# Kernel tuning notes

Hardware: AMD Instinct MI355X
Metric: run time of the kernel (lower is better)

The kernel has to match this reference:

```python
import jax, jax.numpy as jnp
import numpy as np

B, T, H, V = 256, 256, 512, 32000
L = 3  # stacked LSTM layers


def setup_inputs() -> dict:
    key = jax.random.key(0)
    ks = jax.random.split(key, 12)
    s = 0.05
    n = lambda k, shp: (jax.random.normal(k, shp, jnp.float32) * s)
    return {
        "text_1": jax.random.randint(ks[0], (B, T), 0, V, dtype=jnp.int32),
        "text_2": jax.random.randint(ks[1], (B, T), 0, V, dtype=jnp.int32),
        "text_3": jax.random.randint(ks[2], (B, T), 0, V, dtype=jnp.int32),
        "emb": n(ks[3], (V, H)),
        "Wx": n(ks[4], (L, H, 4 * H)),
        "Wh": n(ks[5], (L, H, 4 * H)),
        "b": jnp.zeros((L, 4 * H), jnp.float32),
        "g1": jnp.ones((3 * H,), jnp.float32), "beta1": jnp.zeros((3 * H,), jnp.float32),
        "W1": n(ks[6], (3 * H, 2 * H)), "bd1": jnp.zeros((2 * H,), jnp.float32),
        "g2": jnp.ones((2 * H,), jnp.float32), "beta2": jnp.zeros((2 * H,), jnp.float32),
        "W2": n(ks[7], (2 * H, H // 5)), "bd2": jnp.zeros((H // 5,), jnp.float32),
        "g3": jnp.ones((H // 5,), jnp.float32), "beta3": jnp.zeros((H // 5,), jnp.float32),
        "W3": n(ks[8], (H // 5, 4)), "bd3": jnp.zeros((4,), jnp.float32),
    }


def _lstm_stack(tokens, emb, Wx, Wh, b):
    # tokens: [B, T] int -> last hidden of top layer [B, H]
    x = emb[tokens]                      # [B, T, H]
    x = jnp.transpose(x, (1, 0, 2))      # [T, B, H] (scan over time)
    bsz, h = x.shape[1], Wh.shape[1]
    for l in range(Wx.shape[0]):
        Wx_l, Wh_l, b_l = Wx[l], Wh[l], b[l]
        def step(carry, xt):
            hprev, cprev = carry
            gates = xt @ Wx_l + hprev @ Wh_l + b_l      # [B, 4H]
            i, f, g, o = jnp.split(gates, 4, axis=-1)
            c = jax.nn.sigmoid(f) * cprev + jax.nn.sigmoid(i) * jnp.tanh(g)
            hnew = jax.nn.sigmoid(o) * jnp.tanh(c)
            return (hnew, c), hnew
        init = (jnp.zeros((bsz, h), x.dtype), jnp.zeros((bsz, h), x.dtype))
        _, x = jax.lax.scan(step, init, x)
    return x[-1]                          # rnn_output[:, -1, :]


def _bn(x, gamma, beta, eps=1e-3):
    m = jnp.mean(x, axis=0)
    v = jnp.var(x, axis=0)
    return gamma * (x - m) * jax.lax.rsqrt(v + eps) + beta


def reference(text_1, text_2, text_3, emb, Wx, Wh, b,
              g1, beta1, W1, bd1, g2, beta2, W2, bd2, g3, beta3, W3, bd3):
    r1 = _lstm_stack(text_1, emb, Wx, Wh, b)
    r2 = _lstm_stack(text_2, emb, Wx, Wh, b)
    r3 = _lstm_stack(text_3, emb, Wx, Wh, b)
    r = jnp.concatenate([r1, r2, r3], axis=1)   # [B, 3H]
    r = _bn(r, g1, beta1)
    r = jax.nn.selu(r @ W1 + bd1)
    r = _bn(r, g2, beta2)
    r = jax.nn.selu(r @ W2 + bd2)
    r = _bn(r, g3, beta3)
    return r @ W3 + bd3                          # [B, 4] logits
```

## Files before the change

### kernel.cpp

```cpp
#include <hip/hip_runtime.h>
#include <hip/hip_bf16.h>
#include <hip/hip_cooperative_groups.h>

namespace cg = cooperative_groups;

typedef __attribute__((ext_vector_type(8))) short short8;
typedef __attribute__((ext_vector_type(4))) float floatx4;

namespace {
constexpr int kB1 = 256;
constexpr int kT  = 256;
constexpr int kH  = 512;
constexpr int kL  = 3;
constexpr int kK  = 1024;
constexpr int kN  = 2048;
constexpr int kGrid = 576;
constexpr size_t kHB = (size_t)768 * kH;

constexpr size_t WREP_OFF   = 0;
constexpr size_t WREP_BYTES = (size_t)kL * kK * kN * 2;
constexpr size_t BREP_OFF   = WREP_OFF + WREP_BYTES;
constexpr size_t BREP_BYTES = (size_t)kL * kN * 4;
constexpr size_t HBUF_OFF   = BREP_OFF + BREP_BYTES;
constexpr size_t HBUF_BYTES = (size_t)kL * 2 * kHB * 2;
constexpr size_t CBUF_OFF   = HBUF_OFF + HBUF_BYTES;
constexpr size_t CBUF_BYTES = (size_t)kL * kHB * 4;
constexpr size_t BNA_OFF    = CBUF_OFF + CBUF_BYTES;
constexpr size_t BNC_OFF    = BNA_OFF + 1536 * 4;
constexpr size_t Z1_OFF     = BNC_OFF + 1536 * 4;
constexpr size_t Z2_OFF     = Z1_OFF + (size_t)256 * 1024 * 4;
constexpr size_t FLAG_OFF   = Z2_OFF + (size_t)256 * 102 * 4;
}

__device__ __forceinline__ float ldf(const void* p, size_t idx, int isf32) {
  if (isf32) return ((const float*)p)[idx];
  return __bfloat162float(((const __hip_bfloat16*)p)[idx]);
}

__device__ __forceinline__ short f2bs(float x) {
  union { __hip_bfloat16 h; short s; } u;
  u.h = __float2bfloat16(x);
  return u.s;
}

__device__ __forceinline__ float fast_tanh(float x) {
  float e = __expf(2.f * x);
  return __fdividef(e - 1.f, e + 1.f);
}
__device__ __forceinline__ float fast_sigmoid(float x) {
  return __fdividef(1.f, 1.f + __expf(-x));
}

__global__ void detect_kernel(const unsigned* __restrict__ g1, int* __restrict__ flag) {
  if (threadIdx.x == 0 && blockIdx.x == 0)
    *flag = (g1[0] == 0x3F800000u) ? 1 : 0;
}

__device__ __forceinline__ void repack_body(
    int start, int stride,
    const void* __restrict__ Wx, const void* __restrict__ Wh,
    const void* __restrict__ bias, int isf32,
    __hip_bfloat16* __restrict__ Wrep, float* __restrict__ brep) {
  for (int idx = start; idx < kL * kK * kN; idx += stride) {
    int j  = idx & 7;
    int n2 = (idx >> 3) & (kN - 1);
    int kg = (idx >> 14) & 127;
    int l  = idx >> 21;
    int k  = kg * 8 + j;
    int ntile = n2 >> 7, c = n2 & 127, g = c >> 5, ul = c & 31;
    int u = ntile * 32 + ul;
    int col = g * 512 + u;
    float v;
    if (k < kH) v = ldf(Wx, ((size_t)l * kH + k) * kN + col, isf32);
    else        v = ldf(Wh, ((size_t)l * kH + (k - kH)) * kN + col, isf32);
    Wrep[idx] = __float2bfloat16(v);
    if (kg == 0 && j == 0) brep[l * kN + n2] = ldf(bias, (size_t)l * kN + col, isf32);
  }
}

__global__ __launch_bounds__(256) void repack_kernel(
    const void* __restrict__ Wx, const void* __restrict__ Wh,
    const void* __restrict__ bias, const int* __restrict__ flagp,
    __hip_bfloat16* __restrict__ Wrep, float* __restrict__ brep) {
  repack_body(blockIdx.x * 256 + threadIdx.x, gridDim.x * 256, Wx, Wh, bias, *flagp,
              Wrep, brep);
}

__device__ __forceinline__ void lstm_step(
    int l, int mt, int nt, int t, int isf32,
    const __hip_bfloat16* __restrict__ WB, float bv0, float bv1,
    __hip_bfloat16* __restrict__ hbuf, float* __restrict__ cl,
    const void* __restrict__ emb, const int* __restrict__ txt,
    char* smem) {
  const int tid = threadIdx.x;
  const int wv = tid >> 6, lane = tid & 63;
  const int lm = lane & 15, lq = lane >> 4;
  const int arow = tid >> 2;
  const int kc   = tid & 3;
  const int row_g = mt * 64 + arow;
  const int n0w = nt * 128 + wv * 32;

  const void* xsrc;  bool xf32 = false;
  if (l == 0) {
    int tok = txt[t];
    if (isf32) { xsrc = (const void*)((const float*)emb + (size_t)tok * kH); xf32 = true; }
    else         xsrc = (const void*)((const __hip_bfloat16*)emb + (size_t)tok * kH);
  } else {
    const __hip_bfloat16* hIn = hbuf + ((size_t)(l - 1) * 2 + (t & 1)) * kHB;
    xsrc = (const void*)(hIn + (size_t)row_g * kH);
  }
  const __hip_bfloat16* hrow = nullptr;
  if (t > 0) {
    const __hip_bfloat16* hPrev = hbuf + ((size_t)l * 2 + ((t & 1) ^ 1)) * kHB;
    hrow = hPrev + (size_t)row_g * kH;
  }

  floatx4 zf = {0.f, 0.f, 0.f, 0.f};
  floatx4 acc[4][2];
#pragma unroll
  for (int a = 0; a < 4; a++)
#pragma unroll
    for (int b = 0; b < 2; b++) acc[a][b] = zf;

#pragma unroll 1
  for (int sl = 0; sl < 8; sl++) {
    short8 bfrag[4][2];
#pragma unroll
    for (int kk = 0; kk < 4; kk++)
#pragma unroll
      for (int nf = 0; nf < 2; nf++) {
        size_t kg = (size_t)(sl * 16 + kk * 4 + lq);
        const __hip_bfloat16* p = WB + (kg * kN + (n0w + nf * 16 + lm)) * 8;
        bfrag[kk][nf] = *(const short8*)p;
      }
    short8 av[4];
    bool zero = (sl >= 4) && (t == 0);
    if (!zero) {
      if (sl < 4 && xf32) {
        const float* sf = (const float*)xsrc + sl * 128;
#pragma unroll
        for (int jj = 0; jj < 4; jj++) {
          const float* q = sf + kc * 8 + jj * 32;
          float4 lo = *(const float4*)q;
          float4 hi = *(const float4*)(q + 4);
          short8 v;
          v[0] = f2bs(lo.x); v[1] = f2bs(lo.y); v[2] = f2bs(lo.z); v[3] = f2bs(lo.w);
          v[4] = f2bs(hi.x); v[5] = f2bs(hi.y); v[6] = f2bs(hi.z); v[7] = f2bs(hi.w);
          av[jj] = v;
        }
      } else {
        const __hip_bfloat16* src = (sl < 4)
            ? ((const __hip_bfloat16*)xsrc + sl * 128)
            : (hrow + (sl - 4) * 128);
#pragma unroll
        for (int jj = 0; jj < 4; jj++)
          av[jj] = *(const short8*)(src + kc * 8 + jj * 32);
      }
    } else {
      short8 vz = {0, 0, 0, 0, 0, 0, 0, 0};
#pragma unroll
      for (int jj = 0; jj < 4; jj++) av[jj] = vz;
    }
    __syncthreads();
#pragma unroll
    for (int jj = 0; jj < 4; jj++) {
      int klocal = kc * 8 + jj * 32;
      *(short8*)(smem + arow * 272 + klocal * 2) = av[jj];
    }
    __syncthreads();
#pragma unroll
    for (int kk = 0; kk < 4; kk++) {
      short8 afrag[4];
#pragma unroll
      for (int mf = 0; mf < 4; mf++) {
        int rowf = mf * 16 + lm;
        afrag[mf] = *(const short8*)(smem + rowf * 272 + kk * 64 + lq * 16);
      }
#pragma unroll
      for (int mf = 0; mf < 4; mf++)
#pragma unroll
        for (int nf = 0; nf < 2; nf++)
          acc[mf][nf] = __builtin_amdgcn_mfma_f32_16x16x32_bf16(
              afrag[mf], bfrag[kk][nf], acc[mf][nf], 0, 0, 0);
    }
  }

#pragma unroll
  for (int mf = 0; mf < 4; mf++)
#pragma unroll
    for (int r = 0; r < 4; r++) {
      acc[mf][0][r] += bv0;
      acc[mf][1][r] += bv1;
    }

  __syncthreads();
  float* gl = (float*)smem;
#pragma unroll
  for (int mf = 0; mf < 4; mf++)
#pragma unroll
    for (int nf = 0; nf < 2; nf++)
#pragma unroll
      for (int r = 0; r < 4; r++) {
        int rowf = mf * 16 + lq * 4 + r;
        int uu   = nf * 16 + lm;
        gl[((size_t)wv * 64 + rowf) * 34 + uu] = acc[mf][nf][r];
      }
  __syncthreads();

  __hip_bfloat16* hout = hbuf + ((size_t)l * 2 + (t & 1)) * kHB;
#pragma unroll
  for (int ii = 0; ii < 8; ii++) {
    int idx = tid + 256 * ii;
    int uu = idx & 31, rowf = idx >> 5;
    float gi = fminf(fmaxf(gl[(0 * 64 + rowf) * 34 + uu], -40.f), 40.f);
    float gf = fminf(fmaxf(gl[(1 * 64 + rowf) * 34 + uu], -40.f), 40.f);
    float gG = fminf(fmaxf(gl[(2 * 64 + rowf) * 34 + uu], -40.f), 40.f);
    float go = fminf(fmaxf(gl[(3 * 64 + rowf) * 34 + uu], -40.f), 40.f);
    int bg = mt * 64 + rowf;
    int ug = nt * 32 + uu;
    size_t off = (size_t)bg * kH + ug;
    float c_old = (t > 0) ? cl[off] : 0.f;
    float cn = fast_sigmoid(gf) * c_old + fast_sigmoid(gi) * fast_tanh(gG);
    float hn = fast_sigmoid(go) * fast_tanh(cn);
    cl[off] = cn;
    hout[off] = __float2bfloat16(hn);
  }
  __syncthreads();
}

__global__ __launch_bounds__(256, 3) void persist_kernel(
    const void* __restrict__ Wx, const void* __restrict__ Wh,
    const void* __restrict__ bias, const int* __restrict__ flagp,
    __hip_bfloat16* __restrict__ Wrep, float* __restrict__ brep,
    __hip_bfloat16* __restrict__ hbuf, float* __restrict__ cbuf,
    const void* __restrict__ emb,
    const int* __restrict__ t1, const int* __restrict__ t2, const int* __restrict__ t3) {
  cg::grid_group gg = cg::this_grid();
  __shared__ __align__(16) char smem[34816];

  const int bid = blockIdx.x;
  const int tid = threadIdx.x;
  const int isf32 = *flagp;

  repack_body(bid * 256 + tid, kGrid * 256, Wx, Wh, bias, isf32, Wrep, brep);
  gg.sync();

  const int l  = bid / 192;
  const int rr = bid % 192;
  const int nt = rr & 15;
  const int mt = rr >> 4;
  const __hip_bfloat16* const WB = Wrep + (size_t)l * kK * kN;
  float* const cl = cbuf + (size_t)l * kHB;
  const int n0w = nt * 128 + (tid >> 6) * 32;
  const int lm = tid & 15;
  const float bv0 = brep[l * kN + n0w + lm];
  const float bv1 = brep[l * kN + n0w + 16 + lm];

  const int* txt = nullptr;
  if (l == 0) {
    int row_g = mt * 64 + (tid >> 2);
    int i = row_g >> 8;
    txt = (i == 0) ? t1 : (i == 1) ? t2 : t3;
    txt += (row_g & 255) * kT;
  }

  for (int s = 0; s < kT + kL - 1; s++) {
    const int t = s - l;
    if (t >= 0 && t < kT)
      lstm_step(l, mt, nt, t, isf32, WB, bv0, bv1, hbuf, cl, emb, txt, smem);
    gg.sync();
  }
}

__global__ __launch_bounds__(256, 3) void step_kernel(
    int s,
    const __hip_bfloat16* __restrict__ Wrep, const float* __restrict__ brep,
    __hip_bfloat16* __restrict__ hbuf, float* __restrict__ cbuf,
    const void* __restrict__ emb, const int* __restrict__ flagp,
    const int* __restrict__ t1, const int* __restrict__ t2, const int* __restrict__ t3) {
  __shared__ __align__(16) char smem[34816];
  const int bid = blockIdx.x;
  const int l  = bid / 192;
  const int rr = bid % 192;
  const int nt = rr & 15;
  const int mt = rr >> 4;
  const int t = s - l;
  if (t < 0 || t >= kT) return;
  const int isf32 = *flagp;
  const int tid = threadIdx.x;
  const __hip_bfloat16* WB = Wrep + (size_t)l * kK * kN;
  float* cl = cbuf + (size_t)l * kHB;
  const int n0w = nt * 128 + (tid >> 6) * 32;
  const int lm = tid & 15;
  const float bv0 = brep[l * kN + n0w + lm];
  const float bv1 = brep[l * kN + n0w + 16 + lm];
  const int* txt = nullptr;
  if (l == 0) {
    int row_g = mt * 64 + (tid >> 2);
    int i = row_g >> 8;
    txt = (i == 0) ? t1 : (i == 1) ? t2 : t3;
    txt += (row_g & 255) * kT;
  }
  lstm_step(l, mt, nt, t, isf32, WB, bv0, bv1, hbuf, cl, emb, txt, smem);
}

__global__ __launch_bounds__(256) void stats_kernel(
    int ncols, int mode, const void* __restrict__ src,
    const void* __restrict__ gamma, const void* __restrict__ beta,
    const int* __restrict__ flagp, float* __restrict__ bn_a, float* __restrict__ bn_c) {
  int isf32 = *flagp;
  int col = blockIdx.x * 256 + threadIdx.x;
  if (col >= ncols) return;
  float sum = 0.f, ss = 0.f;
  for (int b = 0; b < kB1; b++) {
    float v;
    if (mode == 0) {
      const __hip_bfloat16* h = (const __hip_bfloat16*)src;
      v = __bfloat162float(h[((size_t)((col >> 9) * kB1 + b)) * kH + (col & 511)]);
    } else {
      v = ((const float*)src)[(size_t)b * ncols + col];
    }
    v = fmaxf(-1e15f, fminf(v, 1e15f));
    sum += v; ss += v * v;
  }
  float mean = sum * (1.f / kB1);
  float var  = ss * (1.f / kB1) - mean * mean;
  float a = ldf(gamma, col, isf32) * rsqrtf(var + 1e-3f);
  bn_a[col] = a;
  bn_c[col] = ldf(beta, col, isf32) - mean * a;
}

__global__ __launch_bounds__(256) void headgemm_kernel(
    int Kd, int Nd, int mode, const void* __restrict__ Asrc,
    const float* __restrict__ bn_a, const float* __restrict__ bn_c,
    const void* __restrict__ W, const void* __restrict__ bias,
    const int* __restrict__ flagp, float* __restrict__ out, int do_selu) {
  __shared__ float As[32][65];
  __shared__ float Bs[32][65];
  int isf32 = *flagp;
  int tid = threadIdx.x;
  int bx = blockIdx.x, by = blockIdx.y;
  int tx = tid & 15, ty = tid >> 4;
  float acc[4][4] = {};
  int am = tid & 63, ak = tid >> 6;
  int bk = tid >> 3, bn8 = (tid & 7) * 8;
  for (int ks = 0; ks < Kd; ks += 32) {
    __syncthreads();
    for (int jj = 0; jj < 8; jj++) {
      int kl = ak * 8 + jj;
      int kg = ks + kl;
      int mg = by * 64 + am;
      float v;
      if (mode == 0) {
        const __hip_bfloat16* h = (const __hip_bfloat16*)Asrc;
        v = __bfloat162float(h[((size_t)((kg >> 9) * kB1 + mg)) * kH + (kg & 511)]);
      } else {
        v = ((const float*)Asrc)[(size_t)mg * Kd + kg];
      }
      As[kl][am] = v * bn_a[kg] + bn_c[kg];
    }
    for (int e = 0; e < 8; e++) {
      int col = bx * 64 + bn8 + e;
      Bs[bk][bn8 + e] = (col < Nd) ? ldf(W, (size_t)(ks + bk) * Nd + col, isf32) : 0.f;
    }
    __syncthreads();
    for (int k = 0; k < 32; k++) {
      float ar[4], br[4];
#pragma unroll
      for (int i = 0; i < 4; i++) ar[i] = As[k][ty * 4 + i];
#pragma unroll
      for (int j = 0; j < 4; j++) br[j] = Bs[k][tx * 4 + j];
#pragma unroll
      for (int i = 0; i < 4; i++)
#pragma unroll
        for (int j = 0; j < 4; j++) acc[i][j] += ar[i] * br[j];
    }
  }
  for (int i = 0; i < 4; i++) {
    int row = by * 64 + ty * 4 + i;
    for (int j = 0; j < 4; j++) {
      int col = bx * 64 + tx * 4 + j;
      if (col < Nd) {
        float y = acc[i][j] + ldf(bias, col, isf32);
        if (do_selu)
          y = (y > 0.f) ? 1.0507009873554805f * y
                        : 1.0507009873554805f * 1.6732632423543772f * (__expf(y) - 1.f);
        out[(size_t)row * Nd + col] = y;
      }
    }
  }
}

__global__ __launch_bounds__(256) void final_kernel(
    const float* __restrict__ z2, const float* __restrict__ bn_a, const float* __restrict__ bn_c,
    const void* __restrict__ W3, const void* __restrict__ bd3,
    const int* __restrict__ flagp, void* __restrict__ out) {
  int isf32 = *flagp;
  int b = threadIdx.x;
  float acc[4] = {0.f, 0.f, 0.f, 0.f};
  for (int j = 0; j < 102; j++) {
    float y = z2[b * 102 + j] * bn_a[j] + bn_c[j];
#pragma unroll
    for (int g = 0; g < 4; g++) acc[g] += y * ldf(W3, j * 4 + g, isf32);
  }
#pragma unroll
  for (int g = 0; g < 4; g++) {
    float y = acc[g] + ldf(bd3, g, isf32);
    if (isf32) ((float*)out)[b * 4 + g] = y;
    else ((__hip_bfloat16*)out)[b * 4 + g] = __float2bfloat16(y);
  }
}

extern "C" void kernel_launch(void* const* d_in, const int* in_sizes, int n_in,
                              void* d_out, int out_size, void* d_ws, size_t ws_size,
                              hipStream_t stream) {
  const int* t1 = (const int*)d_in[0];
  const int* t2 = (const int*)d_in[1];
  const int* t3 = (const int*)d_in[2];
  const void* emb = d_in[3];
  const void* Wx  = d_in[4];
  const void* Wh  = d_in[5];
  const void* bb  = d_in[6];
  const void* g1  = d_in[7];
  const void* be1 = d_in[8];
  const void* W1  = d_in[9];
  const void* bd1 = d_in[10];
  const void* g2  = d_in[11];
  const void* be2 = d_in[12];
  const void* W2  = d_in[13];
  const void* bd2 = d_in[14];
  const void* g3  = d_in[15];
  const void* be3 = d_in[16];
  const void* W3  = d_in[17];
  const void* bd3 = d_in[18];

  char* ws = (char*)d_ws;
  __hip_bfloat16* Wrep = (__hip_bfloat16*)(ws + WREP_OFF);
  float* brep = (float*)(ws + BREP_OFF);
  __hip_bfloat16* hbuf = (__hip_bfloat16*)(ws + HBUF_OFF);
  float* cbuf = (float*)(ws + CBUF_OFF);
  float* bn_a = (float*)(ws + BNA_OFF);
  float* bn_c = (float*)(ws + BNC_OFF);
  float* z1 = (float*)(ws + Z1_OFF);
  float* z2 = (float*)(ws + Z2_OFF);
  int* flag = (int*)(ws + FLAG_OFF);

  detect_kernel<<<1, 64, 0, stream>>>((const unsigned*)g1, flag);

  bool coop_ok = false;
  {
    int numCU = 0, maxBlk = 0;
    int dev = 0;
    if (hipGetDevice(&dev) == hipSuccess &&
        hipDeviceGetAttribute(&numCU, hipDeviceAttributeMultiprocessorCount, dev) == hipSuccess &&
        hipOccupancyMaxActiveBlocksPerMultiprocessor(&maxBlk, (const void*)persist_kernel,
                                                     256, 0) == hipSuccess) {
      if ((long)maxBlk * numCU >= kGrid) {
        void* args[] = {(void*)&Wx, (void*)&Wh, (void*)&bb, (void*)&flag,
                        (void*)&Wrep, (void*)&brep, (void*)&hbuf, (void*)&cbuf,
                        (void*)&emb, (void*)&t1, (void*)&t2, (void*)&t3};
        hipError_t err = hipLaunchCooperativeKernel((const void*)persist_kernel,
                                                    dim3(kGrid), dim3(256), args, 0, stream);
        if (err == hipSuccess) coop_ok = true;
        else (void)hipGetLastError();
      }
    } else {
      (void)hipGetLastError();
    }
  }
  if (!coop_ok) {
    repack_kernel<<<(kL * kK * kN) / 256, 256, 0, stream>>>(Wx, Wh, bb, flag, Wrep, brep);
    for (int s = 0; s < kT + kL - 1; s++)
      step_kernel<<<kGrid, 256, 0, stream>>>(s, Wrep, brep, hbuf, cbuf, emb, flag, t1, t2, t3);
  }

  const __hip_bfloat16* hTop = hbuf + (2 * 2 + 1) * kHB;
  stats_kernel<<<6, 256, 0, stream>>>(1536, 0, hTop, g1, be1, flag, bn_a, bn_c);
  headgemm_kernel<<<dim3(16, 4), 256, 0, stream>>>(1536, 1024, 0, hTop, bn_a, bn_c, W1, bd1, flag, z1, 1);
  stats_kernel<<<4, 256, 0, stream>>>(1024, 1, z1, g2, be2, flag, bn_a, bn_c);
  headgemm_kernel<<<dim3(2, 4), 256, 0, stream>>>(1024, 102, 1, z1, bn_a, bn_c, W2, bd2, flag, z2, 1);
  stats_kernel<<<1, 256, 0, stream>>>(102, 1, z2, g3, be3, flag, bn_a, bn_c);
  final_kernel<<<1, 256, 0, stream>>>(z2, bn_a, bn_c, W3, bd3, flag, (void*)d_out);
}
```

Baseline: 6.296 ms.

## Double-buffer LDS A tiles and prefetch weights in LSTM step

Restructures the per-step GEMM loop so the A operand is staged through two LDS buffers, with global loads for slice sl+2 and the LDS write for sl+1 overlapping the MFMAs of slice sl. B fragments for the next slice are prefetched one k-chunk at a time. The A tile is stored in an MFMA-fragment-friendly layout, and the previous cell state is loaded early. Two barriers per slice become one lighter barrier that waits only on LDS counters, which adds register pressure and relies on the asm barrier being correct for global memory visibility.

New measurement: 6.522 ms. 3.6% more time.

```diff
diff --git a/kernel.cpp b/kernel.cpp
--- a/kernel.cpp
+++ b/kernel.cpp
@@ -41,6 +41,10 @@
   union { __hip_bfloat16 h; short s; } u;
   u.h = __float2bfloat16(x);
   return u.s;
+}
+
+__device__ __forceinline__ void sync_lds() {
+  asm volatile("s_waitcnt lgkmcnt(0)\n\ts_barrier" ::: "memory");
 }
 
 __device__ __forceinline__ float fast_tanh(float x) {
@@ -93,12 +97,12 @@
     const void* __restrict__ emb, const int* __restrict__ txt,
     char* smem) {
   const int tid = threadIdx.x;
-  const int wv = tid >> 6, lane = tid & 63;
+  const int lane = tid & 63;
   const int lm = lane & 15, lq = lane >> 4;
   const int arow = tid >> 2;
   const int kc   = tid & 3;
   const int row_g = mt * 64 + arow;
-  const int n0w = nt * 128 + wv * 32;
+  const int n0w = nt * 128 + (tid >> 6) * 32;
 
   const void* xsrc;  bool xf32 = false;
   if (l == 0) {
@@ -115,6 +119,73 @@
     hrow = hPrev + (size_t)row_g * kH;
   }
 
+  const int e_uu = tid & 31;
+  const int e_r0 = tid >> 5;
+
+  char* const buf0 = smem;
+  char* const buf1 = smem + 16384;
+  const int abase = ((arow >> 4) * 256 + kc * 16 + (arow & 15)) * 16;
+
+  short8 av[4];
+  short8 bf[4][2];
+
+  auto loadA = [&](int sl) {
+    if ((sl >= 4) && (t == 0)) {
+      short8 vz = {0, 0, 0, 0, 0, 0, 0, 0};
+#pragma unroll
+      for (int jj = 0; jj < 4; jj++) av[jj] = vz;
+    } else if (sl < 4 && xf32) {
+      const float* sf = (const float*)xsrc + sl * 128;
+#pragma unroll
+      for (int jj = 0; jj < 4; jj++) {
+        const float* q = sf + kc * 8 + jj * 32;
+        float4 lo = *(const float4*)q;
+        float4 hi = *(const float4*)(q + 4);
+        short8 v;
+        v[0] = f2bs(lo.x); v[1] = f2bs(lo.y); v[2] = f2bs(lo.z); v[3] = f2bs(lo.w);
+        v[4] = f2bs(hi.x); v[5] = f2bs(hi.y); v[6] = f2bs(hi.z); v[7] = f2bs(hi.w);
+        av[jj] = v;
+      }
+    } else {
+      const __hip_bfloat16* src = (sl < 4)
+          ? ((const __hip_bfloat16*)xsrc + sl * 128)
+          : (hrow + (sl - 4) * 128);
+#pragma unroll
+      for (int jj = 0; jj < 4; jj++)
+        av[jj] = *(const short8*)(src + kc * 8 + jj * 32);
+    }
+  };
+  auto writeA = [&](char* b) {
+#pragma unroll
+    for (int jj = 0; jj < 4; jj++)
+      *(short8*)(b + abase + jj * 1024) = av[jj];
+  };
+  auto loadBfrag = [&](int sl, int kk) {
+#pragma unroll
+    for (int nf = 0; nf < 2; nf++) {
+      size_t kg = (size_t)(sl * 16 + kk * 4 + lq);
+      bf[kk][nf] = *(const short8*)(WB + (kg * kN + (n0w + nf * 16 + lm)) * 8);
+    }
+  };
+
+  loadA(0);
+#pragma unroll
+  for (int kk = 0; kk < 4; kk++) loadBfrag(0, kk);
+  writeA(buf0);
+  loadA(1);
+  float cold[8];
+  if (t > 0) {
+#pragma unroll
+    for (int ii = 0; ii < 8; ii++) {
+      int rowf = e_r0 + 8 * ii;
+      cold[ii] = cl[(size_t)(mt * 64 + rowf) * kH + nt * 32 + e_uu];
+    }
+  } else {
+#pragma unroll
+    for (int ii = 0; ii < 8; ii++) cold[ii] = 0.f;
+  }
+  sync_lds();
+
   floatx4 zf = {0.f, 0.f, 0.f, 0.f};
   floatx4 acc[4][2];
 #pragma unroll
@@ -124,65 +195,25 @@
 
 #pragma unroll 1
   for (int sl = 0; sl < 8; sl++) {
-    short8 bfrag[4][2];
-#pragma unroll
-    for (int kk = 0; kk < 4; kk++)
-#pragma unroll
-      for (int nf = 0; nf < 2; nf++) {
-        size_t kg = (size_t)(sl * 16 + kk * 4 + lq);
-        const __hip_bfloat16* p = WB + (kg * kN + (n0w + nf * 16 + lm)) * 8;
-        bfrag[kk][nf] = *(const short8*)p;
-      }
-    short8 av[4];
-    bool zero = (sl >= 4) && (t == 0);
-    if (!zero) {
-      if (sl < 4 && xf32) {
-        const float* sf = (const float*)xsrc + sl * 128;
-#pragma unroll
-        for (int jj = 0; jj < 4; jj++) {
-          const float* q = sf + kc * 8 + jj * 32;
-          float4 lo = *(const float4*)q;
-          float4 hi = *(const float4*)(q + 4);
-          short8 v;
-          v[0] = f2bs(lo.x); v[1] = f2bs(lo.y); v[2] = f2bs(lo.z); v[3] = f2bs(lo.w);
-          v[4] = f2bs(hi.x); v[5] = f2bs(hi.y); v[6] = f2bs(hi.z); v[7] = f2bs(hi.w);
-          av[jj] = v;
-        }
-      } else {
-        const __hip_bfloat16* src = (sl < 4)
-            ? ((const __hip_bfloat16*)xsrc + sl * 128)
-            : (hrow + (sl - 4) * 128);
-#pragma unroll
-        for (int jj = 0; jj < 4; jj++)
-          av[jj] = *(const short8*)(src + kc * 8 + jj * 32);
-      }
-    } else {
-      short8 vz = {0, 0, 0, 0, 0, 0, 0, 0};
-#pragma unroll
-      for (int jj = 0; jj < 4; jj++) av[jj] = vz;
-    }
-    __syncthreads();
-#pragma unroll
-    for (int jj = 0; jj < 4; jj++) {
-      int klocal = kc * 8 + jj * 32;
-      *(short8*)(smem + arow * 272 + klocal * 2) = av[jj];
-    }
-    __syncthreads();
+    char* const cur = (sl & 1) ? buf1 : buf0;
+    char* const nxt = (sl & 1) ? buf0 : buf1;
+    if (sl < 7) writeA(nxt);
+    if (sl < 6) loadA(sl + 2);
 #pragma unroll
     for (int kk = 0; kk < 4; kk++) {
       short8 afrag[4];
 #pragma unroll
-      for (int mf = 0; mf < 4; mf++) {
-        int rowf = mf * 16 + lm;
-        afrag[mf] = *(const short8*)(smem + rowf * 272 + kk * 64 + lq * 16);
-      }
+      for (int mf = 0; mf < 4; mf++)
+        afrag[mf] = *(const short8*)(cur + (mf * 4 + kk) * 1024 + lane * 16);
 #pragma unroll
       for (int mf = 0; mf < 4; mf++)
 #pragma unroll
         for (int nf = 0; nf < 2; nf++)
           acc[mf][nf] = __builtin_amdgcn_mfma_f32_16x16x32_bf16(
-              afrag[mf], bfrag[kk][nf], acc[mf][nf], 0, 0, 0);
-    }
+              afrag[mf], bf[kk][nf], acc[mf][nf], 0, 0, 0);
+      if (sl < 7) loadBfrag(sl + 1, kk);
+    }
+    sync_lds();
   }
 
 #pragma unroll
@@ -193,39 +224,38 @@
       acc[mf][1][r] += bv1;
     }
 
-  __syncthreads();
   float* gl = (float*)smem;
-#pragma unroll
-  for (int mf = 0; mf < 4; mf++)
-#pragma unroll
-    for (int nf = 0; nf < 2; nf++)
-#pragma unroll
-      for (int r = 0; r < 4; r++) {
-        int rowf = mf * 16 + lq * 4 + r;
-        int uu   = nf * 16 + lm;
-        gl[((size_t)wv * 64 + rowf) * 34 + uu] = acc[mf][nf][r];
-      }
-  __syncthreads();
+  {
+    const int wv = tid >> 6;
+#pragma unroll
+    for (int mf = 0; mf < 4; mf++)
+#pragma unroll
+      for (int nf = 0; nf < 2; nf++)
+#pragma unroll
+        for (int r = 0; r < 4; r++) {
+          int rowf = mf * 16 + lq * 4 + r;
+          int uu   = nf * 16 + lm;
+          gl[((size_t)wv * 64 + rowf) * 34 + uu] = acc[mf][nf][r];
+        }
+  }
+  sync_lds();
 
   __hip_bfloat16* hout = hbuf + ((size_t)l * 2 + (t & 1)) * kHB;
 #pragma unroll
   for (int ii = 0; ii < 8; ii++) {
-    int idx = tid + 256 * ii;
-    int uu = idx & 31, rowf = idx >> 5;
+    int rowf = e_r0 + 8 * ii;
+    int uu = e_uu;
     float gi = fminf(fmaxf(gl[(0 * 64 + rowf) * 34 + uu], -40.f), 40.f);
     float gf = fminf(fmaxf(gl[(1 * 64 + rowf) * 34 + uu], -40.f), 40.f);
     float gG = fminf(fmaxf(gl[(2 * 64 + rowf) * 34 + uu], -40.f), 40.f);
     float go = fminf(fmaxf(gl[(3 * 64 + rowf) * 34 + uu], -40.f), 40.f);
-    int bg = mt * 64 + rowf;
-    int ug = nt * 32 + uu;
-    size_t off = (size_t)bg * kH + ug;
-    float c_old = (t > 0) ? cl[off] : 0.f;
-    float cn = fast_sigmoid(gf) * c_old + fast_sigmoid(gi) * fast_tanh(gG);
+    size_t off = (size_t)(mt * 64 + rowf) * kH + nt * 32 + uu;
+    float cn = fast_sigmoid(gf) * cold[ii] + fast_sigmoid(gi) * fast_tanh(gG);
     float hn = fast_sigmoid(go) * fast_tanh(cn);
     cl[off] = cn;
     hout[off] = __float2bfloat16(hn);
   }
-  __syncthreads();
+  sync_lds();
 }
 
 __global__ __launch_bounds__(256, 3) void persist_kernel(
```
